# Performance work log

Hardware: AMD Instinct MI355X
Metric: run time of the kernel (lower is better)

## Reference

```python
import jax, jax.numpy as jnp
import numpy as np

B, N, D = 16, 512, 256
PH, UH, UPH = 8, 4, 4          # P_GAT heads, U_GAT heads, UP_GAT heads
P_LAYERS, U_LAYERS = 2, 1
FH, NC = 128, 2                # final hidden, num classes
N_TRAIT = 4


def setup_inputs() -> dict:
    key = jax.random.key(0)
    keys = iter(jax.random.split(key, 64))

    def rn(shape, s=0.05):
        return jax.random.normal(next(keys), shape, dtype=jnp.float32) * s

    inp = {
        "p_mask": jnp.ones((B, N), jnp.float32),
        "feature": rn((B, N, D), 1.0),
        "c_node": rn((B, 1, D), 1.0),
        "pgat_W": rn((D, D)),
        "pgat_attn": rn((PH, 2 * (D // PH))),
    }
    for i in range(1, 5):
        inp[f"up{i}_qw"] = rn((D, D))
        inp[f"up{i}_qb"] = rn((D,))
        inp[f"up{i}_kw"] = rn((D, D))
        inp[f"up{i}_kb"] = rn((D,))
        inp[f"up{i}_ow"] = rn((D, D * UPH))
        inp[f"up{i}_ob"] = rn((D,))
    inp["ugat_W"] = rn((D, D))
    inp["ugat_attn"] = rn((UH, 2 * (D // UH)))
    inp["mlp_w1"] = rn((FH, D))
    inp["mlp_b1"] = rn((FH,))
    inp["mlp_w2"] = rn((FH, FH))
    inp["mlp_b2"] = rn((FH,))
    for i in range(1, 5):
        inp[f"fcf{i}_w"] = rn((NC, FH))
        inp[f"fcf{i}_b"] = rn((NC,))
    return inp


def _mh_gat(feature, W, attn_w, n_head, num_layers, adj=None):
    """Shared math of P_GAT / U_GAT.
    attn(cat([q_i, k_j]))[..., h, h] decomposes into q_i.wq_h + k_j.wk_h,
    identical math to the broadcast-concat-linear-diagonal in the source."""
    Bx, Nx, d = feature.shape
    dh = d // n_head
    wq, wk = attn_w[:, :dh], attn_w[:, dh:]           # [h, dh] each
    for _ in range(num_layers):
        qk = (feature @ W.T).reshape(Bx, Nx, n_head, dh)
        sq = jnp.einsum('bqhd,hd->bqh', qk, wq)
        sk = jnp.einsum('bkhd,hd->bkh', qk, wk)
        scores = jnp.tanh(sq[:, :, None, :] + sk[:, None, :, :])  # [B,q,k,h]
        if adj is not None:
            scores = jnp.where(adj[:, :, :, None] == 0, jnp.float32(-1e-8), scores)
        att = jax.nn.softmax(scores, axis=-2)          # softmax over k
        hid = jnp.tanh(jnp.einsum('bqkh,bkhd->bqhd', att, qk))
        feature = feature + hid.reshape(Bx, Nx, d)
    return feature


def _up_gat(p_mask, p_feat, u_feat, qw, qb, kw, kb, ow, ob):
    """UP_GAT: all heads/layers share params & inputs -> identical heads."""
    d = p_feat.shape[-1]
    q = u_feat @ qw.T + qb                             # [B,1,D]
    k = p_feat @ kw.T + kb                             # [B,Np,D]
    sim = jnp.einsum('bqd,bkd->bqk', q, k) / jnp.sqrt(jnp.float32(d))
    sim = jnp.where(p_mask[:, None, :] == 0, jnp.float32(1e-8), sim)
    att = jax.nn.softmax(sim, axis=2)
    head = att @ p_feat                                # [B,1,D]
    mh = jnp.concatenate([head] * UPH, axis=-1)        # concat of identical heads
    return (mh @ ow.T + ob)[:, 0, :]                   # squeeze(1)


def reference(p_mask, feature, c_node, pgat_W, pgat_attn,
              up1_qw, up1_qb, up1_kw, up1_kb, up1_ow, up1_ob,
              up2_qw, up2_qb, up2_kw, up2_kb, up2_ow, up2_ob,
              up3_qw, up3_qb, up3_kw, up3_kb, up3_ow, up3_ob,
              up4_qw, up4_qb, up4_kw, up4_kb, up4_ow, up4_ob,
              ugat_W, ugat_attn, mlp_w1, mlp_b1, mlp_w2, mlp_b2,
              fcf1_w, fcf1_b, fcf2_w, fcf2_b, fcf3_w, fcf3_b, fcf4_w, fcf4_b):
    Bx = p_mask.shape[0]
    adj = p_mask[:, :, None] * p_mask[:, None, :]      # [B,N,N]
    new_p = _mh_gat(feature, pgat_W, pgat_attn, PH, P_LAYERS, adj=adj)
    new_mask = jnp.concatenate([p_mask, jnp.ones((Bx, 1), p_mask.dtype)], axis=1)
    comb = jnp.concatenate([new_p, c_node], axis=1)    # [B,N+1,D]

    u1 = _up_gat(new_mask, comb, c_node, up1_qw, up1_qb, up1_kw, up1_kb, up1_ow, up1_ob)
    u2 = _up_gat(new_mask, comb, c_node, up2_qw, up2_qb, up2_kw, up2_kb, up2_ow, up2_ob)
    u3 = _up_gat(new_mask, comb, c_node, up3_qw, up3_qb, up3_kw, up3_kb, up3_ow, up3_ob)
    u4 = _up_gat(new_mask, comb, c_node, up4_qw, up4_qb, up4_kw, up4_kb, up4_ow, up4_ob)

    u = jnp.stack([u1, u2, u3, u4], axis=1)            # [B,4,D]
    u = _mh_gat(u, ugat_W, ugat_attn, UH, U_LAYERS, adj=None)

    def mlp(x):  # fcs1..4 share modules in the torch source
        h = jax.nn.relu(x @ mlp_w1.T + mlp_b1)
        return jax.nn.relu(h @ mlp_w2.T + mlp_b2)

    heads = [(fcf1_w, fcf1_b), (fcf2_w, fcf2_b), (fcf3_w, fcf3_b), (fcf4_w, fcf4_b)]
    logits = [mlp(u[:, i]) @ w.T + b for i, (w, b) in enumerate(heads)]
    return jnp.stack(logits, axis=0)                   # [4,B,NC]
```

## Files before the change

### kernel.cpp

```cpp
#include <hip/hip_runtime.h>

constexpr int CB   = 16;
constexpr int CN   = 512;
constexpr int CD   = 256;
constexpr int CPH  = 8;
constexpr int CDH  = 32;
constexpr int CNP1 = 513;
constexpr int CFH  = 128;
constexpr int CNC  = 2;

typedef __bf16 bf16x8 __attribute__((ext_vector_type(8)));
typedef __bf16 bf16x4 __attribute__((ext_vector_type(4)));
typedef float  f32x4  __attribute__((ext_vector_type(4)));

__device__ __forceinline__ float tanh_fast(float x) {
  x = fminf(fmaxf(x, -15.f), 15.f);
  float e = __expf(2.f * x);
  return (e - 1.f) / (e + 1.f);
}

__device__ __forceinline__ float exp2x_clamped(float x) {
  x = fminf(fmaxf(x, -18.f), 18.f);
  return __expf(2.f * x);
}

__global__ __launch_bounds__(256) void gemm_fused(
    const float* __restrict__ A, const float* __restrict__ W,
    const float* __restrict__ attnw, __bf16* __restrict__ C,
    float* __restrict__ sqT, float* __restrict__ skT)
{
  const int t  = threadIdx.x;
  const int nt = blockIdx.x * 64;
  const int mt = blockIdx.y * 64;
  const int wv = t >> 6, ln = t & 63;
  const int quad = ln >> 4, lc = ln & 15;

  __shared__ __align__(16) __bf16 aHi[64][56];
  __shared__ __align__(16) __bf16 aLo[64][56];
  __shared__ __align__(16) __bf16 bHi[64][56];
  __shared__ __align__(16) __bf16 bLo[64][56];

  f32x4 acc[4];
#pragma unroll
  for (int j = 0; j < 4; j++)
#pragma unroll
    for (int r = 0; r < 4; r++) acc[j][r] = 0.f;

  const int sr  = t >> 2;
  const int skq = (t & 3) * 8;

  for (int k0 = 0; k0 < 256; k0 += 32) {
    __syncthreads();
    {
      const float* ap = A + (size_t)(mt + sr) * 256 + k0 + skq;
      const float* wp = W + (size_t)(nt + sr) * 256 + k0 + skq;
      float4 a0 = *(const float4*)ap, a1 = *(const float4*)(ap + 4);
      float4 w0 = *(const float4*)wp, w1 = *(const float4*)(wp + 4);
      float av[8] = {a0.x, a0.y, a0.z, a0.w, a1.x, a1.y, a1.z, a1.w};
      float wvv[8] = {w0.x, w0.y, w0.z, w0.w, w1.x, w1.y, w1.z, w1.w};
      bf16x8 ah, al, bh, bl;
#pragma unroll
      for (int j = 0; j < 8; j++) {
        ah[j] = (__bf16)av[j];
        al[j] = (__bf16)(av[j] - (float)ah[j]);
        bh[j] = (__bf16)wvv[j];
        bl[j] = (__bf16)(wvv[j] - (float)bh[j]);
      }
      *(bf16x8*)&aHi[sr][skq] = ah;
      *(bf16x8*)&aLo[sr][skq] = al;
      *(bf16x8*)&bHi[sr][skq] = bh;
      *(bf16x8*)&bLo[sr][skq] = bl;
    }
    __syncthreads();
    bf16x8 fah = *(const bf16x8*)&aHi[wv * 16 + lc][quad * 8];
    bf16x8 fal = *(const bf16x8*)&aLo[wv * 16 + lc][quad * 8];
#pragma unroll
    for (int j = 0; j < 4; j++) {
      bf16x8 fbh = *(const bf16x8*)&bHi[j * 16 + lc][quad * 8];
      bf16x8 fbl = *(const bf16x8*)&bLo[j * 16 + lc][quad * 8];
      acc[j] = __builtin_amdgcn_mfma_f32_16x16x32_bf16(fah, fbh, acc[j], 0, 0, 0);
      acc[j] = __builtin_amdgcn_mfma_f32_16x16x32_bf16(fah, fbl, acc[j], 0, 0, 0);
      acc[j] = __builtin_amdgcn_mfma_f32_16x16x32_bf16(fal, fbh, acc[j], 0, 0, 0);
    }
  }
#pragma unroll
  for (int j = 0; j < 4; j++)
#pragma unroll
    for (int r = 0; r < 4; r++)
      C[(size_t)(mt + wv * 16 + quad * 4 + r) * 256 + nt + j * 16 + lc] =
          (__bf16)acc[j][r];

  const int hA = blockIdx.x * 2, hB = hA + 1;
  const float wqa0 = attnw[hA * 64 + lc],      wqa1 = attnw[hA * 64 + 16 + lc];
  const float wka0 = attnw[hA * 64 + 32 + lc], wka1 = attnw[hA * 64 + 48 + lc];
  const float wqb0 = attnw[hB * 64 + lc],      wqb1 = attnw[hB * 64 + 16 + lc];
  const float wkb0 = attnw[hB * 64 + 32 + lc], wkb1 = attnw[hB * 64 + 48 + lc];
  float sqa[4], ska[4], sqb[4], skb[4];
#pragma unroll
  for (int r = 0; r < 4; r++) {
    sqa[r] = acc[0][r] * wqa0 + acc[1][r] * wqa1;
    ska[r] = acc[0][r] * wka0 + acc[1][r] * wka1;
    sqb[r] = acc[2][r] * wqb0 + acc[3][r] * wqb1;
    skb[r] = acc[2][r] * wkb0 + acc[3][r] * wkb1;
  }
#pragma unroll
  for (int m = 1; m <= 8; m <<= 1) {
#pragma unroll
    for (int r = 0; r < 4; r++) {
      sqa[r] += __shfl_xor(sqa[r], m);
      ska[r] += __shfl_xor(ska[r], m);
      sqb[r] += __shfl_xor(sqb[r], m);
      skb[r] += __shfl_xor(skb[r], m);
    }
  }
  if (lc == 0) {
#pragma unroll
    for (int r = 0; r < 4; r++) {
      int gm = mt + wv * 16 + quad * 4 + r;
      int bb = gm >> 9, nn = gm & 511;
      sqT[((size_t)bb * CPH + hA) * CN + nn] = sqa[r];
      skT[((size_t)bb * CPH + hA) * CN + nn] = ska[r];
      sqT[((size_t)bb * CPH + hB) * CN + nn] = sqb[r];
      skT[((size_t)bb * CPH + hB) * CN + nn] = skb[r];
    }
  }
}

__global__ __launch_bounds__(256) void pgat_attn_mfma2(
    const __bf16* __restrict__ qk, const float* __restrict__ sqT,
    const float* __restrict__ skT, const float* __restrict__ pmask,
    const float* __restrict__ fin, float* __restrict__ fout, int outStride)
{
  const int qt = blockIdx.x;
  const int h  = blockIdx.y;
  const int b  = blockIdx.z;
  const int t  = threadIdx.x;
  const int wv = t >> 6;
  const int ln = t & 63;
  const int quad = ln >> 4;
  const int lc   = ln & 15;

  __shared__ __align__(16) __bf16 pbuf[128][72];
  __shared__ __align__(16) __bf16 vbuf[32][72];
  __shared__ float skl[CN];
  __shared__ float ckm[CN];
  __shared__ float sql[128];
  __shared__ float qfm[128];

  for (int i = t; i < CN; i += 256) {
    skl[i] = exp2x_clamped(skT[((size_t)b * CPH + h) * CN + i]);
    ckm[i] = (pmask[b * CN + i] == 0.f) ? 0.f : 1.f;
  }
  if (t < 128) {
    sql[t] = exp2x_clamped(sqT[((size_t)b * CPH + h) * CN + qt * 128 + t]);
    qfm[t] = (pmask[b * CN + qt * 128 + t] == 0.f) ? 0.f : 1.f;
  }

  f32x4 aV0 = {0.f,0.f,0.f,0.f}, aV1 = {0.f,0.f,0.f,0.f}, aD = {0.f,0.f,0.f,0.f};
  f32x4 bV0 = {0.f,0.f,0.f,0.f}, bV1 = {0.f,0.f,0.f,0.f}, bD = {0.f,0.f,0.f,0.f};
  bf16x8 ones;
#pragma unroll
  for (int j = 0; j < 8; j++) ones[j] = (__bf16)1.0f;

  const int qg  = t >> 1;
  const int kb  = (t & 1) * 32;
  const int vkk = t >> 3;
  const int vdq = (t & 7) * 4;

  for (int k0 = 0; k0 < CN; k0 += 64) {
    __syncthreads();
    {
      bf16x4 v0 = *(const bf16x4*)(qk + ((size_t)(b * CN + k0 + vkk)) * CD + h * CDH + vdq);
      bf16x4 v1 = *(const bf16x4*)(qk + ((size_t)(b * CN + k0 + 32 + vkk)) * CD + h * CDH + vdq);
      vbuf[vdq + 0][vkk] = v0[0]; vbuf[vdq + 1][vkk] = v0[1];
      vbuf[vdq + 2][vkk] = v0[2]; vbuf[vdq + 3][vkk] = v0[3];
      vbuf[vdq + 0][32 + vkk] = v1[0]; vbuf[vdq + 1][32 + vkk] = v1[1];
      vbuf[vdq + 2][32 + vkk] = v1[2]; vbuf[vdq + 3][32 + vkk] = v1[3];
    }
    {
      const float tq = sql[qg];
      const float qf = qfm[qg];
#pragma unroll
      for (int g = 0; g < 4; g++) {
        bf16x8 w;
#pragma unroll
        for (int j = 0; j < 8; j++) {
          const int kk = k0 + kb + g * 8 + j;
          float u  = tq * skl[kk];
          float th = (u - 1.f) * __builtin_amdgcn_rcpf(u + 1.f);
          th *= qf * ckm[kk];
          w[j] = (__bf16)__expf(th);
        }
        *(bf16x8*)&pbuf[qg][kb + g * 8] = w;
      }
    }
    __syncthreads();
#pragma unroll
    for (int s = 0; s < 2; s++) {
      bf16x8 b0 = *(const bf16x8*)&vbuf[lc][s * 32 + quad * 8];
      bf16x8 b1 = *(const bf16x8*)&vbuf[16 + lc][s * 32 + quad * 8];
      bf16x8 fa = *(const bf16x8*)&pbuf[wv * 16 + lc][s * 32 + quad * 8];
      bf16x8 fb = *(const bf16x8*)&pbuf[64 + wv * 16 + lc][s * 32 + quad * 8];
      aV0 = __builtin_amdgcn_mfma_f32_16x16x32_bf16(fa, b0, aV0, 0, 0, 0);
      aV1 = __builtin_amdgcn_mfma_f32_16x16x32_bf16(fa, b1, aV1, 0, 0, 0);
      aD  = __builtin_amdgcn_mfma_f32_16x16x32_bf16(fa, ones, aD, 0, 0, 0);
      bV0 = __builtin_amdgcn_mfma_f32_16x16x32_bf16(fb, b0, bV0, 0, 0, 0);
      bV1 = __builtin_amdgcn_mfma_f32_16x16x32_bf16(fb, b1, bV1, 0, 0, 0);
      bD  = __builtin_amdgcn_mfma_f32_16x16x32_bf16(fb, ones, bD, 0, 0, 0);
    }
  }
#pragma unroll
  for (int r = 0; r < 4; r++) {
    const int d0 = h * CDH + lc;
    {
      int q = qt * 128 + wv * 16 + quad * 4 + r;
      float inv = 1.f / aD[r];
      const float* ip = fin + ((size_t)b * CN + q) * CD;
      float*       op = fout + ((size_t)b * outStride + q) * CD;
      op[d0]      = ip[d0]      + tanh_fast(aV0[r] * inv);
      op[d0 + 16] = ip[d0 + 16] + tanh_fast(aV1[r] * inv);
    }
    {
      int q = qt * 128 + 64 + wv * 16 + quad * 4 + r;
      float inv = 1.f / bD[r];
      const float* ip = fin + ((size_t)b * CN + q) * CD;
      float*       op = fout + ((size_t)b * outStride + q) * CD;
      op[d0]      = ip[d0]      + tanh_fast(bV0[r] * inv);
      op[d0 + 16] = ip[d0 + 16] + tanh_fast(bV1[r] * inv);
    }
  }
}


__global__ __launch_bounds__(256) void up_q_all(
    const float* __restrict__ cnode,
    const float* __restrict__ qw0, const float* __restrict__ qb0,
    const float* __restrict__ kw0, const float* __restrict__ kb0,
    const float* __restrict__ ow0,
    const float* __restrict__ qw1, const float* __restrict__ qb1,
    const float* __restrict__ kw1, const float* __restrict__ kb1,
    const float* __restrict__ ow1,
    const float* __restrict__ qw2, const float* __restrict__ qb2,
    const float* __restrict__ kw2, const float* __restrict__ kb2,
    const float* __restrict__ ow2,
    const float* __restrict__ qw3, const float* __restrict__ qb3,
    const float* __restrict__ kw3, const float* __restrict__ kb3,
    const float* __restrict__ ow3,
    float* __restrict__ qt_, float* __restrict__ qkb,
    float* __restrict__ comb, float* __restrict__ head, float* __restrict__ den,
    float* __restrict__ weff)
{
  const int up = blockIdx.x, b = blockIdx.y, t = threadIdx.x;
  const float* qw = (up == 0) ? qw0 : (up == 1) ? qw1 : (up == 2) ? qw2 : qw3;
  const float* qb = (up == 0) ? qb0 : (up == 1) ? qb1 : (up == 2) ? qb2 : qb3;
  const float* kw = (up == 0) ? kw0 : (up == 1) ? kw1 : (up == 2) ? kw2 : kw3;
  const float* kb = (up == 0) ? kb0 : (up == 1) ? kb1 : (up == 2) ? kb2 : kb3;
  const float* ow = (up == 0) ? ow0 : (up == 1) ? ow1 : (up == 2) ? ow2 : ow3;
  __shared__ float cl[CD];
  __shared__ float ql[CD];
  __shared__ float red[256];
  cl[t] = cnode[b * CD + t];
  head[((size_t)b * 4 + up) * CD + t] = 0.f;
  if (t == 0) den[b * 4 + up] = 0.f;

  {
#pragma unroll
    for (int i = 0; i < 4; i++) {
      int idx = t + 256 * i;
      int n = b * 16 + (idx >> 6), e4 = (idx & 63) * 4;
      const float* base = ow + (size_t)n * (4 * CD) + e4;
      float4 w0 = *(const float4*)(base);
      float4 w1 = *(const float4*)(base + CD);
      float4 w2 = *(const float4*)(base + 2 * CD);
      float4 w3 = *(const float4*)(base + 3 * CD);
      float4 o;
      o.x = w0.x + w1.x + w2.x + w3.x;
      o.y = w0.y + w1.y + w2.y + w3.y;
      o.z = w0.z + w1.z + w2.z + w3.z;
      o.w = w0.w + w1.w + w2.w + w3.w;
      *(float4*)(weff + (size_t)up * CD * CD + (size_t)n * CD + e4) = o;
    }
  }
  __syncthreads();
  if (up == 0) comb[((size_t)b * CNP1 + CN) * CD + t] = cl[t];
  {
    const float* wr = qw + (size_t)t * CD;
    float a = qb[t];
#pragma unroll 4
    for (int k = 0; k < CD; k += 4) {
      float4 w4 = *(const float4*)(wr + k);
      a += cl[k] * w4.x + cl[k + 1] * w4.y + cl[k + 2] * w4.z + cl[k + 3] * w4.w;
    }
    ql[t] = a;
  }
  __syncthreads();
  {
    float a0 = 0.f, a1 = 0.f, a2 = 0.f, a3 = 0.f;
#pragma unroll 4
    for (int d = 0; d < CD; d += 4) {
      a0 += ql[d]     * kw[(d)     * CD + t];
      a1 += ql[d + 1] * kw[(d + 1) * CD + t];
      a2 += ql[d + 2] * kw[(d + 2) * CD + t];
      a3 += ql[d + 3] * kw[(d + 3) * CD + t];
    }
    qt_[((size_t)up * CB + b) * CD + t] = (a0 + a1) + (a2 + a3);
  }
  red[t] = ql[t] * kb[t];
  __syncthreads();
  for (int s = 128; s > 0; s >>= 1) { if (t < s) red[t] += red[t + s]; __syncthreads(); }
  if (t == 0) qkb[up * CB + b] = red[0];
}

__global__ __launch_bounds__(256) void up_headsim(
    const float* __restrict__ comb, const float* __restrict__ qt,
    const float* __restrict__ qkb, const float* __restrict__ pmask,
    float* __restrict__ head, float* __restrict__ den)
{
  const int b = blockIdx.x, n0 = blockIdx.y * 64, t = threadIdx.x;
  const int up = t >> 6, j = t & 63;
  __shared__ float qtl[4][CD];
  __shared__ float qkbl[4];
  __shared__ float attl[4][64];
  for (int i = t; i < 4 * CD; i += 256)
    qtl[i >> 8][i & 255] = qt[((size_t)(i >> 8) * CB + b) * CD + (i & 255)];
  if (t < 4) qkbl[t] = qkb[t * CB + b];
  __syncthreads();
  {
    const int n = n0 + j;
    float e = 0.f;
    if (n < CNP1) {
      const float* cr = comb + ((size_t)b * CNP1 + n) * CD;
      float p = 0.f;
#pragma unroll 4
      for (int d = 0; d < CD; d += 4) {
        float4 c4 = *(const float4*)(cr + d);
        p += qtl[up][d] * c4.x + qtl[up][d + 1] * c4.y
           + qtl[up][d + 2] * c4.z + qtl[up][d + 3] * c4.w;
      }
      float s = (p + qkbl[up]) * 0.0625f;
      float m = (n < CN) ? pmask[b * CN + n] : 1.f;
      if (m == 0.f) s = 1e-8f;
      e = __expf(s);
    }
    attl[up][j] = e;
  }
  __syncthreads();
  float4 acc = make_float4(0.f, 0.f, 0.f, 0.f);
  const int nmax = min(64, CNP1 - n0);
  for (int jj = 0; jj < nmax; jj++) {
    float a = attl[up][jj];
    float4 c4 = *(const float4*)(comb + ((size_t)b * CNP1 + n0 + jj) * CD + j * 4);
    acc.x += a * c4.x; acc.y += a * c4.y; acc.z += a * c4.z; acc.w += a * c4.w;
  }
  float* hp = head + ((size_t)b * 4 + up) * CD + j * 4;
  atomicAdd(hp + 0, acc.x); atomicAdd(hp + 1, acc.y);
  atomicAdd(hp + 2, acc.z); atomicAdd(hp + 3, acc.w);
  if (j == 0) {
    float s = 0.f;
    for (int jj = 0; jj < 64; jj++) s += attl[up][jj];
    atomicAdd(den + b * 4 + up, s);
  }
}

__global__ __launch_bounds__(256) void up_out_ugat(
    const float* __restrict__ head, const float* __restrict__ den,
    const float* __restrict__ weff,
    const float* __restrict__ ob0, const float* __restrict__ ob1,
    const float* __restrict__ ob2, const float* __restrict__ ob3,
    const float* __restrict__ ugat_W, const float* __restrict__ attnw,
    float* __restrict__ uout, float* __restrict__ uqk, float* __restrict__ sqk)
{
  const int b = blockIdx.x, up = blockIdx.y, t = threadIdx.x;
  const float* ob = (up == 0) ? ob0 : (up == 1) ? ob1 : (up == 2) ? ob2 : ob3;
  __shared__ float hl[CD];
  __shared__ float xl[CD];
  __shared__ float qkl[CD];
  hl[t] = head[((size_t)b * 4 + up) * CD + t] * (1.f / den[b * 4 + up]);
  __syncthreads();
  {
    const float* r0 = weff + (size_t)up * CD * CD + (size_t)t * CD;
    float p0 = 0.f, p1 = 0.f, p2 = 0.f, p3 = 0.f;
#pragma unroll 4
    for (int d = 0; d < CD; d += 16) {
      float4 w0 = *(const float4*)(r0 + d);
      float4 w1 = *(const float4*)(r0 + d + 4);
      float4 w2 = *(const float4*)(r0 + d + 8);
      float4 w3 = *(const float4*)(r0 + d + 12);
      p0 += hl[d +  0] * w0.x + hl[d +  1] * w0.y + hl[d +  2] * w0.z + hl[d +  3] * w0.w;
      p1 += hl[d +  4] * w1.x + hl[d +  5] * w1.y + hl[d +  6] * w1.z + hl[d +  7] * w1.w;
      p2 += hl[d +  8] * w2.x + hl[d +  9] * w2.y + hl[d + 10] * w2.z + hl[d + 11] * w2.w;
      p3 += hl[d + 12] * w3.x + hl[d + 13] * w3.y + hl[d + 14] * w3.z + hl[d + 15] * w3.w;
    }
    float a = ob[t] + ((p0 + p1) + (p2 + p3));
    xl[t] = a;
    uout[((size_t)b * 4 + up) * CD + t] = a;
  }
  __syncthreads();
  {
    const float* wr = ugat_W + (size_t)t * CD;
    float p0 = 0.f, p1 = 0.f, p2 = 0.f, p3 = 0.f;
#pragma unroll 4
    for (int d = 0; d < CD; d += 16) {
      float4 w0 = *(const float4*)(wr + d);
      float4 w1 = *(const float4*)(wr + d + 4);
      float4 w2 = *(const float4*)(wr + d + 8);
      float4 w3 = *(const float4*)(wr + d + 12);
      p0 += xl[d +  0] * w0.x + xl[d +  1] * w0.y + xl[d +  2] * w0.z + xl[d +  3] * w0.w;
      p1 += xl[d +  4] * w1.x + xl[d +  5] * w1.y + xl[d +  6] * w1.z + xl[d +  7] * w1.w;
      p2 += xl[d +  8] * w2.x + xl[d +  9] * w2.y + xl[d + 10] * w2.z + xl[d + 11] * w2.w;
      p3 += xl[d + 12] * w3.x + xl[d + 13] * w3.y + xl[d + 14] * w3.z + xl[d + 15] * w3.w;
    }
    float a = (p0 + p1) + (p2 + p3);
    qkl[t] = a;
    uqk[((size_t)b * 4 + up) * CD + t] = a;
  }
  __syncthreads();
  if (t < 8) {
    const int h = t >> 1, which = t & 1;
    const float* w = attnw + h * 128 + which * 64;
    float s = 0.f;
    for (int j = 0; j < 64; j++) s += qkl[h * 64 + j] * w[j];
    sqk[(((size_t)b * 4 + up) * 4 + h) * 2 + which] = s;
  }
}

__global__ __launch_bounds__(256) void ugat_mlp2(
    const float* __restrict__ u, const float* __restrict__ uqk,
    const float* __restrict__ sqk,
    const float* __restrict__ w1, const float* __restrict__ b1,
    const float* __restrict__ w2, const float* __restrict__ b2,
    const float* __restrict__ f1w, const float* __restrict__ f1b,
    const float* __restrict__ f2w, const float* __restrict__ f2b,
    const float* __restrict__ f3w, const float* __restrict__ f3b,
    const float* __restrict__ f4w, const float* __restrict__ f4b,
    float* __restrict__ out)
{
  const int b = blockIdx.x, trait = blockIdx.y, t = threadIdx.x;
  __shared__ float uq[4][CD];
  __shared__ float sl[4][4], kl[4][4];
  __shared__ float xl[CD];
  __shared__ float h1[CFH];
  __shared__ float h2[CFH];
  for (int i = t; i < 4 * CD; i += 256) uq[i >> 8][i & 255] = uqk[(size_t)b * 4 * CD + i];
  if (t < 16) {
    int node = t >> 2, h = t & 3;
    sl[node][h] = sqk[(((size_t)b * 4 + node) * 4 + h) * 2 + 0];
    kl[node][h] = sqk[(((size_t)b * 4 + node) * 4 + h) * 2 + 1];
  }
  float ur = u[((size_t)b * 4 + trait) * CD + t];
  __syncthreads();
  {
    const int h = t >> 6;
    float e[4]; float ssum = 0.f;
#pragma unroll
    for (int k = 0; k < 4; k++) { e[k] = __expf(tanh_fast(sl[trait][h] + kl[k][h])); ssum += e[k]; }
    float hid = 0.f;
#pragma unroll
    for (int k = 0; k < 4; k++) hid += e[k] * uq[k][t];
    xl[t] = ur + tanh_fast(hid / ssum);
  }
  __syncthreads();
  if (t < CFH) {
    const float* r = w1 + (size_t)t * CD;
    float a = b1[t];
#pragma unroll 4
    for (int k = 0; k < CD; k += 4) {
      float4 v = *(const float4*)(r + k);
      a += xl[k] * v.x + xl[k + 1] * v.y + xl[k + 2] * v.z + xl[k + 3] * v.w;
    }
    h1[t] = fmaxf(a, 0.f);
  }
  __syncthreads();
  if (t < CFH) {
    const float* r = w2 + (size_t)t * CFH;
    float a = b2[t];
#pragma unroll 4
    for (int k = 0; k < CFH; k += 4) {
      float4 v = *(const float4*)(r + k);
      a += h1[k] * v.x + h1[k + 1] * v.y + h1[k + 2] * v.z + h1[k + 3] * v.w;
    }
    h2[t] = fmaxf(a, 0.f);
  }
  __syncthreads();
  if (t < CNC) {
    const float* fw; const float* fb;
    switch (trait) {
      case 0:  fw = f1w; fb = f1b; break;
      case 1:  fw = f2w; fb = f2b; break;
      case 2:  fw = f3w; fb = f3b; break;
      default: fw = f4w; fb = f4b; break;
    }
    const float* r = fw + (size_t)t * CFH;
    float a = fb[t];
    for (int k = 0; k < CFH; k++) a += h2[k] * r[k];
    out[(size_t)trait * (CB * CNC) + b * CNC + t] = a;
  }
}

extern "C" void kernel_launch(void* const* d_in, const int* in_sizes, int n_in,
                              void* d_out, int out_size, void* d_ws, size_t ws_size,
                              hipStream_t stream) {
  (void)in_sizes; (void)n_in; (void)out_size; (void)ws_size;
  const float* pmask    = (const float*)d_in[0];
  const float* feature  = (const float*)d_in[1];
  const float* cnode    = (const float*)d_in[2];
  const float* pgat_W   = (const float*)d_in[3];
  const float* pgat_att = (const float*)d_in[4];
  const float* upw[4][6];
  for (int i = 0; i < 4; i++)
    for (int j = 0; j < 6; j++) upw[i][j] = (const float*)d_in[5 + i * 6 + j];
  const float* ugat_W   = (const float*)d_in[29];
  const float* ugat_att = (const float*)d_in[30];
  const float* mlp_w1 = (const float*)d_in[31];
  const float* mlp_b1 = (const float*)d_in[32];
  const float* mlp_w2 = (const float*)d_in[33];
  const float* mlp_b2 = (const float*)d_in[34];
  const float* fcf[8];
  for (int j = 0; j < 8; j++) fcf[j] = (const float*)d_in[35 + j];

  float* ws = (float*)d_ws;
  size_t o = 0;
  float* ws_qk   = ws + o; o += (size_t)CB * CN * CD;
  float* ws_feat = ws + o; o += (size_t)CB * CN * CD;
  float* ws_comb = ws + o; o += (size_t)CB * CNP1 * CD;
  float* ws_sq   = ws + o; o += (size_t)CB * CPH * CN;
  float* ws_sk   = ws + o; o += (size_t)CB * CPH * CN;
  float* ws_qt   = ws + o; o += (size_t)4 * CB * CD;
  float* ws_qkb  = ws + o; o += 4 * CB;
  float* ws_den  = ws + o; o += CB * 4;
  float* ws_head = ws + o; o += (size_t)CB * 4 * CD;
  float* ws_u    = ws + o; o += (size_t)CB * 4 * CD;
  float* ws_uqk  = ws + o; o += (size_t)CB * 4 * CD;
  float* ws_sqk  = ws + o; o += (size_t)CB * 4 * 4 * 2;
  float* ws_weff = ws + o; o += (size_t)4 * CD * CD;
  __bf16* qk16 = (__bf16*)ws_qk;

  const dim3 gemmGrid(CD / 64, (CB * CN) / 64);
  const dim3 attnGrid(CN / 128, CPH, CB);

  gemm_fused<<<gemmGrid, 256, 0, stream>>>(feature, pgat_W, pgat_att, qk16, ws_sq, ws_sk);
  pgat_attn_mfma2<<<attnGrid, 256, 0, stream>>>(qk16, ws_sq, ws_sk, pmask, feature, ws_feat, CN);
  gemm_fused<<<gemmGrid, 256, 0, stream>>>(ws_feat, pgat_W, pgat_att, qk16, ws_sq, ws_sk);
  pgat_attn_mfma2<<<attnGrid, 256, 0, stream>>>(qk16, ws_sq, ws_sk, pmask, ws_feat, ws_comb, CNP1);

  up_q_all<<<dim3(4, CB), 256, 0, stream>>>(cnode,
      upw[0][0], upw[0][1], upw[0][2], upw[0][3], upw[0][4],
      upw[1][0], upw[1][1], upw[1][2], upw[1][3], upw[1][4],
      upw[2][0], upw[2][1], upw[2][2], upw[2][3], upw[2][4],
      upw[3][0], upw[3][1], upw[3][2], upw[3][3], upw[3][4],
      ws_qt, ws_qkb, ws_comb, ws_head, ws_den, ws_weff);
  up_headsim<<<dim3(CB, (CNP1 + 63) / 64), 256, 0, stream>>>(ws_comb, ws_qt, ws_qkb, pmask,
                                                             ws_head, ws_den);
  up_out_ugat<<<dim3(CB, 4), 256, 0, stream>>>(ws_head, ws_den, ws_weff,
      upw[0][5], upw[1][5], upw[2][5], upw[3][5],
      ugat_W, ugat_att, ws_u, ws_uqk, ws_sqk);

  ugat_mlp2<<<dim3(CB, 4), 256, 0, stream>>>(ws_u, ws_uqk, ws_sqk,
                                             mlp_w1, mlp_b1, mlp_w2, mlp_b2,
                                             fcf[0], fcf[1], fcf[2], fcf[3],
                                             fcf[4], fcf[5], fcf[6], fcf[7],
                                             (float*)d_out);
}
```

Baseline: 276.1 us.

## Fold UP-query prep into first GEMM launch and merge UGAT with MLP kernel

The up_q_all work (query projection, key folding, W_eff head-sum) now runs as 16 extra block rows appended to the first gemm_fused grid, so it shares a launch with the P_GAT projection. The separate up_out_ugat and ugat_mlp2 kernels are merged into one 1024-thread block per batch that handles all four traits. The u, uqk and sqk intermediates now stay in shared memory instead of global memory. This removes two kernel launches and their global round trips. In exchange, the GEMM kernel's shared-memory footprint grows, and the merged tail kernel runs only 16 large blocks.

```diff
diff --git a/kernel.cpp b/kernel.cpp
--- a/kernel.cpp
+++ b/kernel.cpp
@@ -27,212 +27,7 @@
 __global__ __launch_bounds__(256) void gemm_fused(
     const float* __restrict__ A, const float* __restrict__ W,
     const float* __restrict__ attnw, __bf16* __restrict__ C,
-    float* __restrict__ sqT, float* __restrict__ skT)
-{
-  const int t  = threadIdx.x;
-  const int nt = blockIdx.x * 64;
-  const int mt = blockIdx.y * 64;
-  const int wv = t >> 6, ln = t & 63;
-  const int quad = ln >> 4, lc = ln & 15;
-
-  __shared__ __align__(16) __bf16 aHi[64][56];
-  __shared__ __align__(16) __bf16 aLo[64][56];
-  __shared__ __align__(16) __bf16 bHi[64][56];
-  __shared__ __align__(16) __bf16 bLo[64][56];
-
-  f32x4 acc[4];
-#pragma unroll
-  for (int j = 0; j < 4; j++)
-#pragma unroll
-    for (int r = 0; r < 4; r++) acc[j][r] = 0.f;
-
-  const int sr  = t >> 2;
-  const int skq = (t & 3) * 8;
-
-  for (int k0 = 0; k0 < 256; k0 += 32) {
-    __syncthreads();
-    {
-      const float* ap = A + (size_t)(mt + sr) * 256 + k0 + skq;
-      const float* wp = W + (size_t)(nt + sr) * 256 + k0 + skq;
-      float4 a0 = *(const float4*)ap, a1 = *(const float4*)(ap + 4);
-      float4 w0 = *(const float4*)wp, w1 = *(const float4*)(wp + 4);
-      float av[8] = {a0.x, a0.y, a0.z, a0.w, a1.x, a1.y, a1.z, a1.w};
-      float wvv[8] = {w0.x, w0.y, w0.z, w0.w, w1.x, w1.y, w1.z, w1.w};
-      bf16x8 ah, al, bh, bl;
-#pragma unroll
-      for (int j = 0; j < 8; j++) {
-        ah[j] = (__bf16)av[j];
-        al[j] = (__bf16)(av[j] - (float)ah[j]);
-        bh[j] = (__bf16)wvv[j];
-        bl[j] = (__bf16)(wvv[j] - (float)bh[j]);
-      }
-      *(bf16x8*)&aHi[sr][skq] = ah;
-      *(bf16x8*)&aLo[sr][skq] = al;
-      *(bf16x8*)&bHi[sr][skq] = bh;
-      *(bf16x8*)&bLo[sr][skq] = bl;
-    }
-    __syncthreads();
-    bf16x8 fah = *(const bf16x8*)&aHi[wv * 16 + lc][quad * 8];
-    bf16x8 fal = *(const bf16x8*)&aLo[wv * 16 + lc][quad * 8];
-#pragma unroll
-    for (int j = 0; j < 4; j++) {
-      bf16x8 fbh = *(const bf16x8*)&bHi[j * 16 + lc][quad * 8];
-      bf16x8 fbl = *(const bf16x8*)&bLo[j * 16 + lc][quad * 8];
-      acc[j] = __builtin_amdgcn_mfma_f32_16x16x32_bf16(fah, fbh, acc[j], 0, 0, 0);
-      acc[j] = __builtin_amdgcn_mfma_f32_16x16x32_bf16(fah, fbl, acc[j], 0, 0, 0);
-      acc[j] = __builtin_amdgcn_mfma_f32_16x16x32_bf16(fal, fbh, acc[j], 0, 0, 0);
-    }
-  }
-#pragma unroll
-  for (int j = 0; j < 4; j++)
-#pragma unroll
-    for (int r = 0; r < 4; r++)
-      C[(size_t)(mt + wv * 16 + quad * 4 + r) * 256 + nt + j * 16 + lc] =
-          (__bf16)acc[j][r];
-
-  const int hA = blockIdx.x * 2, hB = hA + 1;
-  const float wqa0 = attnw[hA * 64 + lc],      wqa1 = attnw[hA * 64 + 16 + lc];
-  const float wka0 = attnw[hA * 64 + 32 + lc], wka1 = attnw[hA * 64 + 48 + lc];
-  const float wqb0 = attnw[hB * 64 + lc],      wqb1 = attnw[hB * 64 + 16 + lc];
-  const float wkb0 = attnw[hB * 64 + 32 + lc], wkb1 = attnw[hB * 64 + 48 + lc];
-  float sqa[4], ska[4], sqb[4], skb[4];
-#pragma unroll
-  for (int r = 0; r < 4; r++) {
-    sqa[r] = acc[0][r] * wqa0 + acc[1][r] * wqa1;
-    ska[r] = acc[0][r] * wka0 + acc[1][r] * wka1;
-    sqb[r] = acc[2][r] * wqb0 + acc[3][r] * wqb1;
-    skb[r] = acc[2][r] * wkb0 + acc[3][r] * wkb1;
-  }
-#pragma unroll
-  for (int m = 1; m <= 8; m <<= 1) {
-#pragma unroll
-    for (int r = 0; r < 4; r++) {
-      sqa[r] += __shfl_xor(sqa[r], m);
-      ska[r] += __shfl_xor(ska[r], m);
-      sqb[r] += __shfl_xor(sqb[r], m);
-      skb[r] += __shfl_xor(skb[r], m);
-    }
-  }
-  if (lc == 0) {
-#pragma unroll
-    for (int r = 0; r < 4; r++) {
-      int gm = mt + wv * 16 + quad * 4 + r;
-      int bb = gm >> 9, nn = gm & 511;
-      sqT[((size_t)bb * CPH + hA) * CN + nn] = sqa[r];
-      skT[((size_t)bb * CPH + hA) * CN + nn] = ska[r];
-      sqT[((size_t)bb * CPH + hB) * CN + nn] = sqb[r];
-      skT[((size_t)bb * CPH + hB) * CN + nn] = skb[r];
-    }
-  }
-}
-
-__global__ __launch_bounds__(256) void pgat_attn_mfma2(
-    const __bf16* __restrict__ qk, const float* __restrict__ sqT,
-    const float* __restrict__ skT, const float* __restrict__ pmask,
-    const float* __restrict__ fin, float* __restrict__ fout, int outStride)
-{
-  const int qt = blockIdx.x;
-  const int h  = blockIdx.y;
-  const int b  = blockIdx.z;
-  const int t  = threadIdx.x;
-  const int wv = t >> 6;
-  const int ln = t & 63;
-  const int quad = ln >> 4;
-  const int lc   = ln & 15;
-
-  __shared__ __align__(16) __bf16 pbuf[128][72];
-  __shared__ __align__(16) __bf16 vbuf[32][72];
-  __shared__ float skl[CN];
-  __shared__ float ckm[CN];
-  __shared__ float sql[128];
-  __shared__ float qfm[128];
-
-  for (int i = t; i < CN; i += 256) {
-    skl[i] = exp2x_clamped(skT[((size_t)b * CPH + h) * CN + i]);
-    ckm[i] = (pmask[b * CN + i] == 0.f) ? 0.f : 1.f;
-  }
-  if (t < 128) {
-    sql[t] = exp2x_clamped(sqT[((size_t)b * CPH + h) * CN + qt * 128 + t]);
-    qfm[t] = (pmask[b * CN + qt * 128 + t] == 0.f) ? 0.f : 1.f;
-  }
-
-  f32x4 aV0 = {0.f,0.f,0.f,0.f}, aV1 = {0.f,0.f,0.f,0.f}, aD = {0.f,0.f,0.f,0.f};
-  f32x4 bV0 = {0.f,0.f,0.f,0.f}, bV1 = {0.f,0.f,0.f,0.f}, bD = {0.f,0.f,0.f,0.f};
-  bf16x8 ones;
-#pragma unroll
-  for (int j = 0; j < 8; j++) ones[j] = (__bf16)1.0f;
-
-  const int qg  = t >> 1;
-  const int kb  = (t & 1) * 32;
-  const int vkk = t >> 3;
-  const int vdq = (t & 7) * 4;
-
-  for (int k0 = 0; k0 < CN; k0 += 64) {
-    __syncthreads();
-    {
-      bf16x4 v0 = *(const bf16x4*)(qk + ((size_t)(b * CN + k0 + vkk)) * CD + h * CDH + vdq);
-      bf16x4 v1 = *(const bf16x4*)(qk + ((size_t)(b * CN + k0 + 32 + vkk)) * CD + h * CDH + vdq);
-      vbuf[vdq + 0][vkk] = v0[0]; vbuf[vdq + 1][vkk] = v0[1];
-      vbuf[vdq + 2][vkk] = v0[2]; vbuf[vdq + 3][vkk] = v0[3];
-      vbuf[vdq + 0][32 + vkk] = v1[0]; vbuf[vdq + 1][32 + vkk] = v1[1];
-      vbuf[vdq + 2][32 + vkk] = v1[2]; vbuf[vdq + 3][32 + vkk] = v1[3];
-    }
-    {
-      const float tq = sql[qg];
-      const float qf = qfm[qg];
-#pragma unroll
-      for (int g = 0; g < 4; g++) {
-        bf16x8 w;
-#pragma unroll
-        for (int j = 0; j < 8; j++) {
-          const int kk = k0 + kb + g * 8 + j;
-          float u  = tq * skl[kk];
-          float th = (u - 1.f) * __builtin_amdgcn_rcpf(u + 1.f);
-          th *= qf * ckm[kk];
-          w[j] = (__bf16)__expf(th);
-        }
-        *(bf16x8*)&pbuf[qg][kb + g * 8] = w;
-      }
-    }
-    __syncthreads();
-#pragma unroll
-    for (int s = 0; s < 2; s++) {
-      bf16x8 b0 = *(const bf16x8*)&vbuf[lc][s * 32 + quad * 8];
-      bf16x8 b1 = *(const bf16x8*)&vbuf[16 + lc][s * 32 + quad * 8];
-      bf16x8 fa = *(const bf16x8*)&pbuf[wv * 16 + lc][s * 32 + quad * 8];
-      bf16x8 fb = *(const bf16x8*)&pbuf[64 + wv * 16 + lc][s * 32 + quad * 8];
-      aV0 = __builtin_amdgcn_mfma_f32_16x16x32_bf16(fa, b0, aV0, 0, 0, 0);
-      aV1 = __builtin_amdgcn_mfma_f32_16x16x32_bf16(fa, b1, aV1, 0, 0, 0);
-      aD  = __builtin_amdgcn_mfma_f32_16x16x32_bf16(fa, ones, aD, 0, 0, 0);
-      bV0 = __builtin_amdgcn_mfma_f32_16x16x32_bf16(fb, b0, bV0, 0, 0, 0);
-      bV1 = __builtin_amdgcn_mfma_f32_16x16x32_bf16(fb, b1, bV1, 0, 0, 0);
-      bD  = __builtin_amdgcn_mfma_f32_16x16x32_bf16(fb, ones, bD, 0, 0, 0);
-    }
-  }
-#pragma unroll
-  for (int r = 0; r < 4; r++) {
-    const int d0 = h * CDH + lc;
-    {
-      int q = qt * 128 + wv * 16 + quad * 4 + r;
-      float inv = 1.f / aD[r];
-      const float* ip = fin + ((size_t)b * CN + q) * CD;
-      float*       op = fout + ((size_t)b * outStride + q) * CD;
-      op[d0]      = ip[d0]      + tanh_fast(aV0[r] * inv);
-      op[d0 + 16] = ip[d0 + 16] + tanh_fast(aV1[r] * inv);
-    }
-    {
-      int q = qt * 128 + 64 + wv * 16 + quad * 4 + r;
-      float inv = 1.f / bD[r];
-      const float* ip = fin + ((size_t)b * CN + q) * CD;
-      float*       op = fout + ((size_t)b * outStride + q) * CD;
-      op[d0]      = ip[d0]      + tanh_fast(bV0[r] * inv);
-      op[d0 + 16] = ip[d0 + 16] + tanh_fast(bV1[r] * inv);
-    }
-  }
-}
-
-
-__global__ __launch_bounds__(256) void up_q_all(
+    float* __restrict__ sqT, float* __restrict__ skT,
     const float* __restrict__ cnode,
     const float* __restrict__ qw0, const float* __restrict__ qb0,
     const float* __restrict__ kw0, const float* __restrict__ kb0,
@@ -250,66 +45,272 @@
     float* __restrict__ comb, float* __restrict__ head, float* __restrict__ den,
     float* __restrict__ weff)
 {
-  const int up = blockIdx.x, b = blockIdx.y, t = threadIdx.x;
-  const float* qw = (up == 0) ? qw0 : (up == 1) ? qw1 : (up == 2) ? qw2 : qw3;
-  const float* qb = (up == 0) ? qb0 : (up == 1) ? qb1 : (up == 2) ? qb2 : qb3;
-  const float* kw = (up == 0) ? kw0 : (up == 1) ? kw1 : (up == 2) ? kw2 : kw3;
-  const float* kb = (up == 0) ? kb0 : (up == 1) ? kb1 : (up == 2) ? kb2 : kb3;
-  const float* ow = (up == 0) ? ow0 : (up == 1) ? ow1 : (up == 2) ? ow2 : ow3;
-  __shared__ float cl[CD];
-  __shared__ float ql[CD];
-  __shared__ float red[256];
-  cl[t] = cnode[b * CD + t];
-  head[((size_t)b * 4 + up) * CD + t] = 0.f;
-  if (t == 0) den[b * 4 + up] = 0.f;
-
-  {
-#pragma unroll
-    for (int i = 0; i < 4; i++) {
-      int idx = t + 256 * i;
-      int n = b * 16 + (idx >> 6), e4 = (idx & 63) * 4;
-      const float* base = ow + (size_t)n * (4 * CD) + e4;
-      float4 w0 = *(const float4*)(base);
-      float4 w1 = *(const float4*)(base + CD);
-      float4 w2 = *(const float4*)(base + 2 * CD);
-      float4 w3 = *(const float4*)(base + 3 * CD);
-      float4 o;
-      o.x = w0.x + w1.x + w2.x + w3.x;
-      o.y = w0.y + w1.y + w2.y + w3.y;
-      o.z = w0.z + w1.z + w2.z + w3.z;
-      o.w = w0.w + w1.w + w2.w + w3.w;
-      *(float4*)(weff + (size_t)up * CD * CD + (size_t)n * CD + e4) = o;
-    }
-  }
-  __syncthreads();
-  if (up == 0) comb[((size_t)b * CNP1 + CN) * CD + t] = cl[t];
-  {
-    const float* wr = qw + (size_t)t * CD;
-    float a = qb[t];
-#pragma unroll 4
-    for (int k = 0; k < CD; k += 4) {
-      float4 w4 = *(const float4*)(wr + k);
-      a += cl[k] * w4.x + cl[k + 1] * w4.y + cl[k + 2] * w4.z + cl[k + 3] * w4.w;
-    }
-    ql[t] = a;
-  }
-  __syncthreads();
-  {
-    float a0 = 0.f, a1 = 0.f, a2 = 0.f, a3 = 0.f;
-#pragma unroll 4
-    for (int d = 0; d < CD; d += 4) {
-      a0 += ql[d]     * kw[(d)     * CD + t];
-      a1 += ql[d + 1] * kw[(d + 1) * CD + t];
-      a2 += ql[d + 2] * kw[(d + 2) * CD + t];
-      a3 += ql[d + 3] * kw[(d + 3) * CD + t];
-    }
-    qt_[((size_t)up * CB + b) * CD + t] = (a0 + a1) + (a2 + a3);
-  }
-  red[t] = ql[t] * kb[t];
-  __syncthreads();
-  for (int s = 128; s > 0; s >>= 1) { if (t < s) red[t] += red[t + s]; __syncthreads(); }
-  if (t == 0) qkb[up * CB + b] = red[0];
-}
+  const int t  = threadIdx.x;
+
+  __shared__ __align__(16) __bf16 aHi[64][56];
+  __shared__ __align__(16) __bf16 aLo[64][56];
+  __shared__ __align__(16) __bf16 bHi[64][56];
+  __shared__ __align__(16) __bf16 bLo[64][56];
+  __shared__ float s_cl[CD];
+  __shared__ float s_ql[CD];
+  __shared__ float s_red[256];
+
+  if (blockIdx.y >= 128) {
+    const int up = blockIdx.x, b = blockIdx.y - 128;
+    const float* qw = (up == 0) ? qw0 : (up == 1) ? qw1 : (up == 2) ? qw2 : qw3;
+    const float* qb = (up == 0) ? qb0 : (up == 1) ? qb1 : (up == 2) ? qb2 : qb3;
+    const float* kw = (up == 0) ? kw0 : (up == 1) ? kw1 : (up == 2) ? kw2 : kw3;
+    const float* kb = (up == 0) ? kb0 : (up == 1) ? kb1 : (up == 2) ? kb2 : kb3;
+    const float* ow = (up == 0) ? ow0 : (up == 1) ? ow1 : (up == 2) ? ow2 : ow3;
+    s_cl[t] = cnode[b * CD + t];
+    head[((size_t)b * 4 + up) * CD + t] = 0.f;
+    if (t == 0) den[b * 4 + up] = 0.f;
+
+    {
+#pragma unroll
+      for (int i = 0; i < 4; i++) {
+        int idx = t + 256 * i;
+        int n = b * 16 + (idx >> 6), e4 = (idx & 63) * 4;
+        const float* base = ow + (size_t)n * (4 * CD) + e4;
+        float4 w0 = *(const float4*)(base);
+        float4 w1 = *(const float4*)(base + CD);
+        float4 w2 = *(const float4*)(base + 2 * CD);
+        float4 w3 = *(const float4*)(base + 3 * CD);
+        float4 o;
+        o.x = w0.x + w1.x + w2.x + w3.x;
+        o.y = w0.y + w1.y + w2.y + w3.y;
+        o.z = w0.z + w1.z + w2.z + w3.z;
+        o.w = w0.w + w1.w + w2.w + w3.w;
+        *(float4*)(weff + (size_t)up * CD * CD + (size_t)n * CD + e4) = o;
+      }
+    }
+    __syncthreads();
+    if (up == 0) comb[((size_t)b * CNP1 + CN) * CD + t] = s_cl[t];
+    {
+      const float* wr = qw + (size_t)t * CD;
+      float a = qb[t];
+#pragma unroll 4
+      for (int k = 0; k < CD; k += 4) {
+        float4 w4 = *(const float4*)(wr + k);
+        a += s_cl[k] * w4.x + s_cl[k + 1] * w4.y + s_cl[k + 2] * w4.z + s_cl[k + 3] * w4.w;
+      }
+      s_ql[t] = a;
+    }
+    __syncthreads();
+    {
+      float a0 = 0.f, a1 = 0.f, a2 = 0.f, a3 = 0.f;
+#pragma unroll 4
+      for (int d = 0; d < CD; d += 4) {
+        a0 += s_ql[d]     * kw[(d)     * CD + t];
+        a1 += s_ql[d + 1] * kw[(d + 1) * CD + t];
+        a2 += s_ql[d + 2] * kw[(d + 2) * CD + t];
+        a3 += s_ql[d + 3] * kw[(d + 3) * CD + t];
+      }
+      qt_[((size_t)up * CB + b) * CD + t] = (a0 + a1) + (a2 + a3);
+    }
+    s_red[t] = s_ql[t] * kb[t];
+    __syncthreads();
+    for (int s = 128; s > 0; s >>= 1) { if (t < s) s_red[t] += s_red[t + s]; __syncthreads(); }
+    if (t == 0) qkb[up * CB + b] = s_red[0];
+    return;
+  }
+
+  const int nt = blockIdx.x * 64;
+  const int mt = blockIdx.y * 64;
+  const int wv = t >> 6, ln = t & 63;
+  const int quad = ln >> 4, lc = ln & 15;
+
+  f32x4 acc[4];
+#pragma unroll
+  for (int j = 0; j < 4; j++)
+#pragma unroll
+    for (int r = 0; r < 4; r++) acc[j][r] = 0.f;
+
+  const int sr  = t >> 2;
+  const int skq = (t & 3) * 8;
+
+  for (int k0 = 0; k0 < 256; k0 += 32) {
+    __syncthreads();
+    {
+      const float* ap = A + (size_t)(mt + sr) * 256 + k0 + skq;
+      const float* wp = W + (size_t)(nt + sr) * 256 + k0 + skq;
+      float4 a0 = *(const float4*)ap, a1 = *(const float4*)(ap + 4);
+      float4 w0 = *(const float4*)wp, w1 = *(const float4*)(wp + 4);
+      float av[8] = {a0.x, a0.y, a0.z, a0.w, a1.x, a1.y, a1.z, a1.w};
+      float wvv[8] = {w0.x, w0.y, w0.z, w0.w, w1.x, w1.y, w1.z, w1.w};
+      bf16x8 ah, al, bh, bl;
+#pragma unroll
+      for (int j = 0; j < 8; j++) {
+        ah[j] = (__bf16)av[j];
+        al[j] = (__bf16)(av[j] - (float)ah[j]);
+        bh[j] = (__bf16)wvv[j];
+        bl[j] = (__bf16)(wvv[j] - (float)bh[j]);
+      }
+      *(bf16x8*)&aHi[sr][skq] = ah;
+      *(bf16x8*)&aLo[sr][skq] = al;
+      *(bf16x8*)&bHi[sr][skq] = bh;
+      *(bf16x8*)&bLo[sr][skq] = bl;
+    }
+    __syncthreads();
+    bf16x8 fah = *(const bf16x8*)&aHi[wv * 16 + lc][quad * 8];
+    bf16x8 fal = *(const bf16x8*)&aLo[wv * 16 + lc][quad * 8];
+#pragma unroll
+    for (int j = 0; j < 4; j++) {
+      bf16x8 fbh = *(const bf16x8*)&bHi[j * 16 + lc][quad * 8];
+      bf16x8 fbl = *(const bf16x8*)&bLo[j * 16 + lc][quad * 8];
+      acc[j] = __builtin_amdgcn_mfma_f32_16x16x32_bf16(fah, fbh, acc[j], 0, 0, 0);
+      acc[j] = __builtin_amdgcn_mfma_f32_16x16x32_bf16(fah, fbl, acc[j], 0, 0, 0);
+      acc[j] = __builtin_amdgcn_mfma_f32_16x16x32_bf16(fal, fbh, acc[j], 0, 0, 0);
+    }
+  }
+#pragma unroll
+  for (int j = 0; j < 4; j++)
+#pragma unroll
+    for (int r = 0; r < 4; r++)
+      C[(size_t)(mt + wv * 16 + quad * 4 + r) * 256 + nt + j * 16 + lc] =
+          (__bf16)acc[j][r];
+
+  const int hA = blockIdx.x * 2, hB = hA + 1;
+  const float wqa0 = attnw[hA * 64 + lc],      wqa1 = attnw[hA * 64 + 16 + lc];
+  const float wka0 = attnw[hA * 64 + 32 + lc], wka1 = attnw[hA * 64 + 48 + lc];
+  const float wqb0 = attnw[hB * 64 + lc],      wqb1 = attnw[hB * 64 + 16 + lc];
+  const float wkb0 = attnw[hB * 64 + 32 + lc], wkb1 = attnw[hB * 64 + 48 + lc];
+  float sqa[4], ska[4], sqb[4], skb[4];
+#pragma unroll
+  for (int r = 0; r < 4; r++) {
+    sqa[r] = acc[0][r] * wqa0 + acc[1][r] * wqa1;
+    ska[r] = acc[0][r] * wka0 + acc[1][r] * wka1;
+    sqb[r] = acc[2][r] * wqb0 + acc[3][r] * wqb1;
+    skb[r] = acc[2][r] * wkb0 + acc[3][r] * wkb1;
+  }
+#pragma unroll
+  for (int m = 1; m <= 8; m <<= 1) {
+#pragma unroll
+    for (int r = 0; r < 4; r++) {
+      sqa[r] += __shfl_xor(sqa[r], m);
+      ska[r] += __shfl_xor(ska[r], m);
+      sqb[r] += __shfl_xor(sqb[r], m);
+      skb[r] += __shfl_xor(skb[r], m);
+    }
+  }
+  if (lc == 0) {
+#pragma unroll
+    for (int r = 0; r < 4; r++) {
+      int gm = mt + wv * 16 + quad * 4 + r;
+      int bb = gm >> 9, nn = gm & 511;
+      sqT[((size_t)bb * CPH + hA) * CN + nn] = sqa[r];
+      skT[((size_t)bb * CPH + hA) * CN + nn] = ska[r];
+      sqT[((size_t)bb * CPH + hB) * CN + nn] = sqb[r];
+      skT[((size_t)bb * CPH + hB) * CN + nn] = skb[r];
+    }
+  }
+}
+
+__global__ __launch_bounds__(256) void pgat_attn_mfma2(
+    const __bf16* __restrict__ qk, const float* __restrict__ sqT,
+    const float* __restrict__ skT, const float* __restrict__ pmask,
+    const float* __restrict__ fin, float* __restrict__ fout, int outStride)
+{
+  const int qt = blockIdx.x;
+  const int h  = blockIdx.y;
+  const int b  = blockIdx.z;
+  const int t  = threadIdx.x;
+  const int wv = t >> 6;
+  const int ln = t & 63;
+  const int quad = ln >> 4;
+  const int lc   = ln & 15;
+
+  __shared__ __align__(16) __bf16 pbuf[128][72];
+  __shared__ __align__(16) __bf16 vbuf[32][72];
+  __shared__ float skl[CN];
+  __shared__ float ckm[CN];
+  __shared__ float sql[128];
+  __shared__ float qfm[128];
+
+  for (int i = t; i < CN; i += 256) {
+    skl[i] = exp2x_clamped(skT[((size_t)b * CPH + h) * CN + i]);
+    ckm[i] = (pmask[b * CN + i] == 0.f) ? 0.f : 1.f;
+  }
+  if (t < 128) {
+    sql[t] = exp2x_clamped(sqT[((size_t)b * CPH + h) * CN + qt * 128 + t]);
+    qfm[t] = (pmask[b * CN + qt * 128 + t] == 0.f) ? 0.f : 1.f;
+  }
+
+  f32x4 aV0 = {0.f,0.f,0.f,0.f}, aV1 = {0.f,0.f,0.f,0.f}, aD = {0.f,0.f,0.f,0.f};
+  f32x4 bV0 = {0.f,0.f,0.f,0.f}, bV1 = {0.f,0.f,0.f,0.f}, bD = {0.f,0.f,0.f,0.f};
+  bf16x8 ones;
+#pragma unroll
+  for (int j = 0; j < 8; j++) ones[j] = (__bf16)1.0f;
+
+  const int qg  = t >> 1;
+  const int kb  = (t & 1) * 32;
+  const int vkk = t >> 3;
+  const int vdq = (t & 7) * 4;
+
+  for (int k0 = 0; k0 < CN; k0 += 64) {
+    __syncthreads();
+    {
+      bf16x4 v0 = *(const bf16x4*)(qk + ((size_t)(b * CN + k0 + vkk)) * CD + h * CDH + vdq);
+      bf16x4 v1 = *(const bf16x4*)(qk + ((size_t)(b * CN + k0 + 32 + vkk)) * CD + h * CDH + vdq);
+      vbuf[vdq + 0][vkk] = v0[0]; vbuf[vdq + 1][vkk] = v0[1];
+      vbuf[vdq + 2][vkk] = v0[2]; vbuf[vdq + 3][vkk] = v0[3];
+      vbuf[vdq + 0][32 + vkk] = v1[0]; vbuf[vdq + 1][32 + vkk] = v1[1];
+      vbuf[vdq + 2][32 + vkk] = v1[2]; vbuf[vdq + 3][32 + vkk] = v1[3];
+    }
+    {
+      const float tq = sql[qg];
+      const float qf = qfm[qg];
+#pragma unroll
+      for (int g = 0; g < 4; g++) {
+        bf16x8 w;
+#pragma unroll
+        for (int j = 0; j < 8; j++) {
+          const int kk = k0 + kb + g * 8 + j;
+          float u  = tq * skl[kk];
+          float th = (u - 1.f) * __builtin_amdgcn_rcpf(u + 1.f);
+          th *= qf * ckm[kk];
+          w[j] = (__bf16)__expf(th);
+        }
+        *(bf16x8*)&pbuf[qg][kb + g * 8] = w;
+      }
+    }
+    __syncthreads();
+#pragma unroll
+    for (int s = 0; s < 2; s++) {
+      bf16x8 b0 = *(const bf16x8*)&vbuf[lc][s * 32 + quad * 8];
+      bf16x8 b1 = *(const bf16x8*)&vbuf[16 + lc][s * 32 + quad * 8];
+      bf16x8 fa = *(const bf16x8*)&pbuf[wv * 16 + lc][s * 32 + quad * 8];
+      bf16x8 fb = *(const bf16x8*)&pbuf[64 + wv * 16 + lc][s * 32 + quad * 8];
+      aV0 = __builtin_amdgcn_mfma_f32_16x16x32_bf16(fa, b0, aV0, 0, 0, 0);
+      aV1 = __builtin_amdgcn_mfma_f32_16x16x32_bf16(fa, b1, aV1, 0, 0, 0);
+      aD  = __builtin_amdgcn_mfma_f32_16x16x32_bf16(fa, ones, aD, 0, 0, 0);
+      bV0 = __builtin_amdgcn_mfma_f32_16x16x32_bf16(fb, b0, bV0, 0, 0, 0);
+      bV1 = __builtin_amdgcn_mfma_f32_16x16x32_bf16(fb, b1, bV1, 0, 0, 0);
+      bD  = __builtin_amdgcn_mfma_f32_16x16x32_bf16(fb, ones, bD, 0, 0, 0);
+    }
+  }
+#pragma unroll
+  for (int r = 0; r < 4; r++) {
+    const int d0 = h * CDH + lc;
+    {
+      int q = qt * 128 + wv * 16 + quad * 4 + r;
+      float inv = 1.f / aD[r];
+      const float* ip = fin + ((size_t)b * CN + q) * CD;
+      float*       op = fout + ((size_t)b * outStride + q) * CD;
+      op[d0]      = ip[d0]      + tanh_fast(aV0[r] * inv);
+      op[d0 + 16] = ip[d0 + 16] + tanh_fast(aV1[r] * inv);
+    }
+    {
+      int q = qt * 128 + 64 + wv * 16 + quad * 4 + r;
+      float inv = 1.f / bD[r];
+      const float* ip = fin + ((size_t)b * CN + q) * CD;
+      float*       op = fout + ((size_t)b * outStride + q) * CD;
+      op[d0]      = ip[d0]      + tanh_fast(bV0[r] * inv);
+      op[d0 + 16] = ip[d0 + 16] + tanh_fast(bV1[r] * inv);
+    }
+  }
+}
+
 
 __global__ __launch_bounds__(256) void up_headsim(
     const float* __restrict__ comb, const float* __restrict__ qt,
@@ -362,71 +363,12 @@
   }
 }
 
-__global__ __launch_bounds__(256) void up_out_ugat(
+__global__ __launch_bounds__(1024) void up_out_mlp(
     const float* __restrict__ head, const float* __restrict__ den,
     const float* __restrict__ weff,
     const float* __restrict__ ob0, const float* __restrict__ ob1,
     const float* __restrict__ ob2, const float* __restrict__ ob3,
     const float* __restrict__ ugat_W, const float* __restrict__ attnw,
-    float* __restrict__ uout, float* __restrict__ uqk, float* __restrict__ sqk)
-{
-  const int b = blockIdx.x, up = blockIdx.y, t = threadIdx.x;
-  const float* ob = (up == 0) ? ob0 : (up == 1) ? ob1 : (up == 2) ? ob2 : ob3;
-  __shared__ float hl[CD];
-  __shared__ float xl[CD];
-  __shared__ float qkl[CD];
-  hl[t] = head[((size_t)b * 4 + up) * CD + t] * (1.f / den[b * 4 + up]);
-  __syncthreads();
-  {
-    const float* r0 = weff + (size_t)up * CD * CD + (size_t)t * CD;
-    float p0 = 0.f, p1 = 0.f, p2 = 0.f, p3 = 0.f;
-#pragma unroll 4
-    for (int d = 0; d < CD; d += 16) {
-      float4 w0 = *(const float4*)(r0 + d);
-      float4 w1 = *(const float4*)(r0 + d + 4);
-      float4 w2 = *(const float4*)(r0 + d + 8);
-      float4 w3 = *(const float4*)(r0 + d + 12);
-      p0 += hl[d +  0] * w0.x + hl[d +  1] * w0.y + hl[d +  2] * w0.z + hl[d +  3] * w0.w;
-      p1 += hl[d +  4] * w1.x + hl[d +  5] * w1.y + hl[d +  6] * w1.z + hl[d +  7] * w1.w;
-      p2 += hl[d +  8] * w2.x + hl[d +  9] * w2.y + hl[d + 10] * w2.z + hl[d + 11] * w2.w;
-      p3 += hl[d + 12] * w3.x + hl[d + 13] * w3.y + hl[d + 14] * w3.z + hl[d + 15] * w3.w;
-    }
-    float a = ob[t] + ((p0 + p1) + (p2 + p3));
-    xl[t] = a;
-    uout[((size_t)b * 4 + up) * CD + t] = a;
-  }
-  __syncthreads();
-  {
-    const float* wr = ugat_W + (size_t)t * CD;
-    float p0 = 0.f, p1 = 0.f, p2 = 0.f, p3 = 0.f;
-#pragma unroll 4
-    for (int d = 0; d < CD; d += 16) {
-      float4 w0 = *(const float4*)(wr + d);
-      float4 w1 = *(const float4*)(wr + d + 4);
-      float4 w2 = *(const float4*)(wr + d + 8);
-      float4 w3 = *(const float4*)(wr + d + 12);
-      p0 += xl[d +  0] * w0.x + xl[d +  1] * w0.y + xl[d +  2] * w0.z + xl[d +  3] * w0.w;
-      p1 += xl[d +  4] * w1.x + xl[d +  5] * w1.y + xl[d +  6] * w1.z + xl[d +  7] * w1.w;
-      p2 += xl[d +  8] * w2.x + xl[d +  9] * w2.y + xl[d + 10] * w2.z + xl[d + 11] * w2.w;
-      p3 += xl[d + 12] * w3.x + xl[d + 13] * w3.y + xl[d + 14] * w3.z + xl[d + 15] * w3.w;
-    }
-    float a = (p0 + p1) + (p2 + p3);
-    qkl[t] = a;
-    uqk[((size_t)b * 4 + up) * CD + t] = a;
-  }
-  __syncthreads();
-  if (t < 8) {
-    const int h = t >> 1, which = t & 1;
-    const float* w = attnw + h * 128 + which * 64;
-    float s = 0.f;
-    for (int j = 0; j < 64; j++) s += qkl[h * 64 + j] * w[j];
-    sqk[(((size_t)b * 4 + up) * 4 + h) * 2 + which] = s;
-  }
-}
-
-__global__ __launch_bounds__(256) void ugat_mlp2(
-    const float* __restrict__ u, const float* __restrict__ uqk,
-    const float* __restrict__ sqk,
     const float* __restrict__ w1, const float* __restrict__ b1,
     const float* __restrict__ w2, const float* __restrict__ b2,
     const float* __restrict__ f1w, const float* __restrict__ f1b,
@@ -435,65 +377,113 @@
     const float* __restrict__ f4w, const float* __restrict__ f4b,
     float* __restrict__ out)
 {
-  const int b = blockIdx.x, trait = blockIdx.y, t = threadIdx.x;
-  __shared__ float uq[4][CD];
-  __shared__ float sl[4][4], kl[4][4];
-  __shared__ float xl[CD];
-  __shared__ float h1[CFH];
-  __shared__ float h2[CFH];
-  for (int i = t; i < 4 * CD; i += 256) uq[i >> 8][i & 255] = uqk[(size_t)b * 4 * CD + i];
-  if (t < 16) {
-    int node = t >> 2, h = t & 3;
-    sl[node][h] = sqk[(((size_t)b * 4 + node) * 4 + h) * 2 + 0];
-    kl[node][h] = sqk[(((size_t)b * 4 + node) * 4 + h) * 2 + 1];
-  }
-  float ur = u[((size_t)b * 4 + trait) * CD + t];
+  const int b = blockIdx.x, t = threadIdx.x;
+  const int g = t >> 8;
+  const int tt = t & 255;
+
+  __shared__ float hl[4][CD];
+  __shared__ float xs[4][CD];
+  __shared__ float uqs[4][CD];
+  __shared__ float sqs[4][4][2];
+  __shared__ float x2[4][CD];
+  __shared__ float h1s[4][CFH];
+  __shared__ float h2s[4][CFH];
+
+  const float* ob = (g == 0) ? ob0 : (g == 1) ? ob1 : (g == 2) ? ob2 : ob3;
+
+  hl[g][tt] = head[((size_t)b * 4 + g) * CD + tt] * (1.f / den[b * 4 + g]);
   __syncthreads();
   {
-    const int h = t >> 6;
+    const float* r0 = weff + (size_t)g * CD * CD + (size_t)tt * CD;
+    float p0 = 0.f, p1 = 0.f, p2 = 0.f, p3 = 0.f;
+#pragma unroll 4
+    for (int d = 0; d < CD; d += 16) {
+      float4 w0 = *(const float4*)(r0 + d);
+      float4 wv1 = *(const float4*)(r0 + d + 4);
+      float4 w2v = *(const float4*)(r0 + d + 8);
+      float4 w3 = *(const float4*)(r0 + d + 12);
+      p0 += hl[g][d +  0] * w0.x + hl[g][d +  1] * w0.y + hl[g][d +  2] * w0.z + hl[g][d +  3] * w0.w;
+      p1 += hl[g][d +  4] * wv1.x + hl[g][d +  5] * wv1.y + hl[g][d +  6] * wv1.z + hl[g][d +  7] * wv1.w;
+      p2 += hl[g][d +  8] * w2v.x + hl[g][d +  9] * w2v.y + hl[g][d + 10] * w2v.z + hl[g][d + 11] * w2v.w;
+      p3 += hl[g][d + 12] * w3.x + hl[g][d + 13] * w3.y + hl[g][d + 14] * w3.z + hl[g][d + 15] * w3.w;
+    }
+    xs[g][tt] = ob[tt] + ((p0 + p1) + (p2 + p3));
+  }
+  __syncthreads();
+  {
+    const float* wr = ugat_W + (size_t)tt * CD;
+    float p0 = 0.f, p1 = 0.f, p2 = 0.f, p3 = 0.f;
+#pragma unroll 4
+    for (int d = 0; d < CD; d += 16) {
+      float4 w0 = *(const float4*)(wr + d);
+      float4 wv1 = *(const float4*)(wr + d + 4);
+      float4 w2v = *(const float4*)(wr + d + 8);
+      float4 w3 = *(const float4*)(wr + d + 12);
+      p0 += xs[g][d +  0] * w0.x + xs[g][d +  1] * w0.y + xs[g][d +  2] * w0.z + xs[g][d +  3] * w0.w;
+      p1 += xs[g][d +  4] * wv1.x + xs[g][d +  5] * wv1.y + xs[g][d +  6] * wv1.z + xs[g][d +  7] * wv1.w;
+      p2 += xs[g][d +  8] * w2v.x + xs[g][d +  9] * w2v.y + xs[g][d + 10] * w2v.z + xs[g][d + 11] * w2v.w;
+      p3 += xs[g][d + 12] * w3.x + xs[g][d + 13] * w3.y + xs[g][d + 14] * w3.z + xs[g][d + 15] * w3.w;
+    }
+    uqs[g][tt] = (p0 + p1) + (p2 + p3);
+  }
+  __syncthreads();
+  if (tt < 8) {
+    const int h = tt >> 1, which = tt & 1;
+    const float* w = attnw + h * 128 + which * 64;
+    float s = 0.f;
+    for (int j = 0; j < 64; j++) s += uqs[g][h * 64 + j] * w[j];
+    sqs[g][h][which] = s;
+  }
+  __syncthreads();
+
+  {
+    const int h = tt >> 6;
     float e[4]; float ssum = 0.f;
 #pragma unroll
-    for (int k = 0; k < 4; k++) { e[k] = __expf(tanh_fast(sl[trait][h] + kl[k][h])); ssum += e[k]; }
+    for (int k = 0; k < 4; k++) {
+      e[k] = __expf(tanh_fast(sqs[g][h][0] + sqs[k][h][1]));
+      ssum += e[k];
+    }
     float hid = 0.f;
 #pragma unroll
-    for (int k = 0; k < 4; k++) hid += e[k] * uq[k][t];
-    xl[t] = ur + tanh_fast(hid / ssum);
-  }
-  __syncthreads();
-  if (t < CFH) {
-    const float* r = w1 + (size_t)t * CD;
-    float a = b1[t];
+    for (int k = 0; k < 4; k++) hid += e[k] * uqs[k][tt];
+    x2[g][tt] = xs[g][tt] + tanh_fast(hid / ssum);
+  }
+  __syncthreads();
+  if (tt < CFH) {
+    const float* r = w1 + (size_t)tt * CD;
+    float a = b1[tt];
 #pragma unroll 4
     for (int k = 0; k < CD; k += 4) {
       float4 v = *(const float4*)(r + k);
-      a += xl[k] * v.x + xl[k + 1] * v.y + xl[k + 2] * v.z + xl[k + 3] * v.w;
-    }
-    h1[t] = fmaxf(a, 0.f);
-  }
-  __syncthreads();
-  if (t < CFH) {
-    const float* r = w2 + (size_t)t * CFH;
-    float a = b2[t];
+      a += x2[g][k] * v.x + x2[g][k + 1] * v.y + x2[g][k + 2] * v.z + x2[g][k + 3] * v.w;
+    }
+    h1s[g][tt] = fmaxf(a, 0.f);
+  }
+  __syncthreads();
+  if (tt < CFH) {
+    const float* r = w2 + (size_t)tt * CFH;
+    float a = b2[tt];
 #pragma unroll 4
     for (int k = 0; k < CFH; k += 4) {
       float4 v = *(const float4*)(r + k);
-      a += h1[k] * v.x + h1[k + 1] * v.y + h1[k + 2] * v.z + h1[k + 3] * v.w;
-    }
-    h2[t] = fmaxf(a, 0.f);
-  }
-  __syncthreads();
-  if (t < CNC) {
+      a += h1s[g][k] * v.x + h1s[g][k + 1] * v.y + h1s[g][k + 2] * v.z + h1s[g][k + 3] * v.w;
+    }
+    h2s[g][tt] = fmaxf(a, 0.f);
+  }
+  __syncthreads();
+  if (tt < CNC) {
     const float* fw; const float* fb;
-    switch (trait) {
+    switch (g) {
       case 0:  fw = f1w; fb = f1b; break;
       case 1:  fw = f2w; fb = f2b; break;
       case 2:  fw = f3w; fb = f3b; break;
       default: fw = f4w; fb = f4b; break;
     }
-    const float* r = fw + (size_t)t * CFH;
-    float a = fb[t];
-    for (int k = 0; k < CFH; k++) a += h2[k] * r[k];
-    out[(size_t)trait * (CB * CNC) + b * CNC + t] = a;
+    const float* r = fw + (size_t)tt * CFH;
+    float a = fb[tt];
+    for (int k = 0; k < CFH; k++) a += h2s[g][k] * r[k];
+    out[(size_t)g * (CB * CNC) + b * CNC + tt] = a;
   }
 }
 
@@ -529,35 +519,37 @@
   float* ws_qkb  = ws + o; o += 4 * CB;
   float* ws_den  = ws + o; o += CB * 4;
   float* ws_head = ws + o; o += (size_t)CB * 4 * CD;
-  float* ws_u    = ws + o; o += (size_t)CB * 4 * CD;
-  float* ws_uqk  = ws + o; o += (size_t)CB * 4 * CD;
-  float* ws_sqk  = ws + o; o += (size_t)CB * 4 * 4 * 2;
   float* ws_weff = ws + o; o += (size_t)4 * CD * CD;
   __bf16* qk16 = (__bf16*)ws_qk;
 
-  const dim3 gemmGrid(CD / 64, (CB * CN) / 64);
+  const dim3 gemmGrid1(CD / 64, (CB * CN) / 64 + 16);
+  const dim3 gemmGrid2(CD / 64, (CB * CN) / 64);
   const dim3 attnGrid(CN / 128, CPH, CB);
 
-  gemm_fused<<<gemmGrid, 256, 0, stream>>>(feature, pgat_W, pgat_att, qk16, ws_sq, ws_sk);
-  pgat_attn_mfma2<<<attnGrid, 256, 0, stream>>>(qk16, ws_sq, ws_sk, pmask, feature, ws_feat, CN);
-  gemm_fused<<<gemmGrid, 256, 0, stream>>>(ws_feat, pgat_W, pgat_att, qk16, ws_sq, ws_sk);
-  pgat_attn_mfma2<<<attnGrid, 256, 0, stream>>>(qk16, ws_sq, ws_sk, pmask, ws_feat, ws_comb, CNP1);
-
-  up_q_all<<<dim3(4, CB), 256, 0, stream>>>(cnode,
+  gemm_fused<<<gemmGrid1, 256, 0, stream>>>(feature, pgat_W, pgat_att, qk16, ws_sq, ws_sk,
+      cnode,
       upw[0][0], upw[0][1], upw[0][2], upw[0][3], upw[0][4],
       upw[1][0], upw[1][1], upw[1][2], upw[1][3], upw[1][4],
       upw[2][0], upw[2][1], upw[2][2], upw[2][3], upw[2][4],
       upw[3][0], upw[3][1], upw[3][2], upw[3][3], upw[3][4],
       ws_qt, ws_qkb, ws_comb, ws_head, ws_den, ws_weff);
+  pgat_attn_mfma2<<<attnGrid, 256, 0, stream>>>(qk16, ws_sq, ws_sk, pmask, feature, ws_feat, CN);
+  gemm_fused<<<gemmGrid2, 256, 0, stream>>>(ws_feat, pgat_W, pgat_att, qk16, ws_sq, ws_sk,
+      cnode,
+      upw[0][0], upw[0][1], upw[0][2], upw[0][3], upw[0][4],
+      upw[1][0], upw[1][1], upw[1][2], upw[1][3], upw[1][4],
+      upw[2][0], upw[2][1], upw[2][2], upw[2][3], upw[2][4],
+      upw[3][0], upw[3][1], upw[3][2], upw[3][3], upw[3][4],
+      ws_qt, ws_qkb, ws_comb, ws_head, ws_den, ws_weff);
+  pgat_attn_mfma2<<<attnGrid, 256, 0, stream>>>(qk16, ws_sq, ws_sk, pmask, ws_feat, ws_comb, CNP1);
+
   up_headsim<<<dim3(CB, (CNP1 + 63) / 64), 256, 0, stream>>>(ws_comb, ws_qt, ws_qkb, pmask,
                                                              ws_head, ws_den);
-  up_out_ugat<<<dim3(CB, 4), 256, 0, stream>>>(ws_head, ws_den, ws_weff,
+  up_out_mlp<<<dim3(CB), 1024, 0, stream>>>(ws_head, ws_den, ws_weff,
       upw[0][5], upw[1][5], upw[2][5], upw[3][5],
-      ugat_W, ugat_att, ws_u, ws_uqk, ws_sqk);
-
-  ugat_mlp2<<<dim3(CB, 4), 256, 0, stream>>>(ws_u, ws_uqk, ws_sqk,
-                                             mlp_w1, mlp_b1, mlp_w2, mlp_b2,
-                                             fcf[0], fcf[1], fcf[2], fcf[3],
-                                             fcf[4], fcf[5], fcf[6], fcf[7],
-                                             (float*)d_out);
-}
+      ugat_W, ugat_att,
+      mlp_w1, mlp_b1, mlp_w2, mlp_b2,
+      fcf[0], fcf[1], fcf[2], fcf[3],
+      fcf[4], fcf[5], fcf[6], fcf[7],
+      (float*)d_out);
+}
```

After: 318.7 us. 15.4% more time.
